# Performance work log

Hardware: AMD Instinct MI355X
Metric: run time of the kernel (lower is better)

The kernel has to match this reference:

```python
import jax, jax.numpy as jnp
import numpy as np

NEG_INF = -1e30
NA_POS = 3  # position of the 'no-answer' token (after [CLS], yes, no)


def mask_pos0(x, mask):
    # keep x where mask==1, set to large negative where mask==0
    return x * mask + (1.0 - mask) * NEG_INF


def make_span_mask(seq_len, max_ans_len):
    m = jnp.tril(jnp.triu(jnp.ones((seq_len, seq_len), jnp.float32), 0), max_ans_len - 1)
    m = m.at[:4, :].set(0.0)
    m = m.at[1, 1].set(1.0)
    m = m.at[2, 2].set(1.0)
    m = m.at[NA_POS, NA_POS].set(1.0)
    return m


def setup_inputs() -> dict:
    key = jax.random.key(0)
    k1, k2, k3 = jax.random.split(key, 3)
    B, S, H = 8, 4096, 1024
    seq_hiddens = jax.random.normal(k1, (B, S, H), jnp.float32)
    ans_mask = jnp.ones((B, S), jnp.float32)
    W_qa = jax.random.normal(k2, (H, 2), jnp.float32) * (1.0 / np.sqrt(H))
    b_qa = jnp.zeros((2,), jnp.float32)
    return {"seq_hiddens": seq_hiddens, "ans_mask": ans_mask, "W_qa": W_qa,
            "b_qa": b_qa, "top_k": 5}


def reference(seq_hiddens, ans_mask, W_qa, b_qa, top_k):
    B, S, H = seq_hiddens.shape
    max_ans_len = 30
    # linear QA head: (B,S,H) @ (H,2) -> (B,S,2)
    span_logits = jnp.einsum('bsh,hc->bsc', seq_hiddens, W_qa) + b_qa
    masked_span_logits = mask_pos0(span_logits, ans_mask[:, :, None])
    start_logits = masked_span_logits[..., 0]  # (B,S)
    end_logits = masked_span_logits[..., 1]    # (B,S)
    # outer-sum span scores: (B,S,S)
    span_scores = start_logits[:, :, None] + end_logits[:, None, :]
    span_mask = make_span_mask(S, max_ans_len)[None]
    masked_span_scores = mask_pos0(span_scores, span_mask)
    flat = masked_span_scores.reshape(B, S * S)
    _, top_span = jax.lax.top_k(flat, top_k)  # (B,k)
    top_start = top_span // S
    top_end = top_span % S
    return start_logits, end_logits, top_start, top_end
```

## Files before the change

kernel.cpp:

```cpp
#include <hip/hip_runtime.h>
#include <cfloat>

#define NEG_INF_F (-1e30f)

__global__ __launch_bounds__(256) void qa_logits_kernel(
    const float* __restrict__ X,
    const float* __restrict__ mask,
    const float* __restrict__ W,
    const float* __restrict__ bqa,
    float* __restrict__ out,
    int total, int H) {
  int wave = (int)((blockIdx.x * (size_t)blockDim.x + threadIdx.x) >> 6);
  int lane = threadIdx.x & 63;
  if (wave >= total) return;
  const float* row = X + (size_t)wave * H;
  float s0 = 0.f, s1 = 0.f;
  int iters = H >> 8;
  for (int k = 0; k < iters; ++k) {
    int h = (k * 64 + lane) * 4;
    const float4 x   = *reinterpret_cast<const float4*>(row + h);
    const float4 w01 = *reinterpret_cast<const float4*>(W + 2 * h);
    const float4 w23 = *reinterpret_cast<const float4*>(W + 2 * h + 4);
    s0 += x.x * w01.x + x.y * w01.z + x.z * w23.x + x.w * w23.z;
    s1 += x.x * w01.y + x.y * w01.w + x.z * w23.y + x.w * w23.w;
  }
#pragma unroll
  for (int off = 32; off > 0; off >>= 1) {
    s0 += __shfl_down(s0, off);
    s1 += __shfl_down(s1, off);
  }
  if (lane == 0) {
    float m = mask[wave];
    float inv = 1.f - m;
    out[wave]         = (s0 + bqa[0]) * m + inv * NEG_INF_F;
    out[total + wave] = (s1 + bqa[1]) * m + inv * NEG_INF_F;
  }
}


__device__ __forceinline__ bool t5_better(float av, int ai, float bv, int bi) {
  return av > bv || (av == bv && ai < bi);
}

__device__ __forceinline__ void t5_insert(float v[5], int id[5], float nv, int ni) {
  if (!t5_better(nv, ni, v[4], id[4])) return;
  v[4] = nv; id[4] = ni;
#pragma unroll
  for (int q = 4; q > 0; --q) {
    if (t5_better(v[q], id[q], v[q - 1], id[q - 1])) {
      float tv = v[q]; v[q] = v[q - 1]; v[q - 1] = tv;
      int ti = id[q]; id[q] = id[q - 1]; id[q - 1] = ti;
    }
  }
}

__device__ __forceinline__ void t5_init(float v[5], int id[5]) {
#pragma unroll
  for (int q = 0; q < 5; ++q) { v[q] = -FLT_MAX; id[q] = 0x7fffffff; }
}

__device__ __forceinline__ void wave_top5(float v[5], int id[5],
                                          float rv[5], int rid[5]) {
#pragma unroll
  for (int r = 0; r < 5; ++r) {
    float bv = v[0]; int bi = id[0];
#pragma unroll
    for (int q = 1; q < 5; ++q)
      if (t5_better(v[q], id[q], bv, bi)) { bv = v[q]; bi = id[q]; }
#pragma unroll
    for (int off = 1; off < 64; off <<= 1) {
      float ov = __shfl_xor(bv, off);
      int oi = __shfl_xor(bi, off);
      if (t5_better(ov, oi, bv, bi)) { bv = ov; bi = oi; }
    }
    rv[r] = bv; rid[r] = bi;
#pragma unroll
    for (int q = 0; q < 5; ++q)
      if (id[q] == bi) v[q] = -FLT_MAX;
  }
}

#define S1_TPB 64

__global__ __launch_bounds__(S1_TPB) void topk_stage1(
    const float* __restrict__ logits,
    float* __restrict__ wv_out,
    int* __restrict__ wi_out,
    int B, int S, int blocks_per_b) {
  int b  = blockIdx.x / blocks_per_b;
  int rb = blockIdx.x % blocks_per_b;
  int lane = (int)threadIdx.x;
  int i = rb * S1_TPB + lane;
  const float* st = logits + (size_t)b * S;
  const float* en = logits + (size_t)(B + b) * S;

  float v[5]; int id[5];
  t5_init(v, id);

  if (i >= 4) {
    float si = st[i];
    float e[30];
#pragma unroll
    for (int c = 0; c < 30; ++c) {
      int j = i + c;
      e[c] = (j < S) ? en[j] : NEG_INF_F;
    }
    int base = i * S + i;
#pragma unroll
    for (int c = 0; c < 30; ++c) t5_insert(v, id, si + e[c], base + c);
  } else if (i >= 1) {
    t5_insert(v, id, st[i] + en[i], i * S + i);
  }

  float rv[5]; int rid[5];
  wave_top5(v, id, rv, rid);

  if (lane == 0) {
    float* ov = wv_out + (size_t)blockIdx.x * 5;
    int*   oi = wi_out + (size_t)blockIdx.x * 5;
#pragma unroll
    for (int q = 0; q < 5; ++q) { ov[q] = rv[q]; oi[q] = rid[q]; }
  }
}

__global__ __launch_bounds__(64) void topk_stage2(
    const float* __restrict__ wv_in, const int* __restrict__ wi_in,
    float* __restrict__ out, int B, int S, int blocks_per_b) {
  int b = blockIdx.x;
  int lane = (int)threadIdx.x;
  int n = blocks_per_b * 5;
  const float* wv = wv_in + (size_t)b * n;
  const int*   wi = wi_in + (size_t)b * n;

  float v[5]; int id[5];
  t5_init(v, id);
#pragma unroll 5
  for (int c = lane; c < n; c += 64)
    t5_insert(v, id, wv[c], wi[c]);

  float rv[5]; int rid[5];
  wave_top5(v, id, rv, rid);

  if (lane == 0) {
    float* ts = out + 2 * (size_t)B * S;
    float* te = ts + (size_t)B * 5;
#pragma unroll
    for (int q = 0; q < 5; ++q) {
      ts[b * 5 + q] = (float)(rid[q] / S);
      te[b * 5 + q] = (float)(rid[q] % S);
    }
  }
}

extern "C" void kernel_launch(void* const* d_in, const int* in_sizes, int n_in,
                              void* d_out, int out_size, void* d_ws, size_t ws_size,
                              hipStream_t stream) {
  const float* X    = (const float*)d_in[0];
  const float* mask = (const float*)d_in[1];
  const float* W    = (const float*)d_in[2];
  const float* bqa  = (const float*)d_in[3];
  const int B = 8, S = 4096, H = 1024;
  const int total = B * S;
  float* out = (float*)d_out;

  int waves_per_block = 256 / 64;
  int blocks = (total + waves_per_block - 1) / waves_per_block;
  qa_logits_kernel<<<blocks, 256, 0, stream>>>(X, mask, W, bqa, out, total, H);

  const int blocks_per_b = S / S1_TPB;
  float* wv_ws = (float*)d_ws;
  int*   wi_ws = (int*)((char*)d_ws + (size_t)B * blocks_per_b * 5 * sizeof(float));
  topk_stage1<<<B * blocks_per_b, S1_TPB, 0, stream>>>(out, wv_ws, wi_ws, B, S, blocks_per_b);
  topk_stage2<<<B, 64, 0, stream>>>(wv_ws, wi_ws, out, B, S, blocks_per_b);
}
```

Measured before the change: 41.77 us.

## Fuse two-stage top-k into one block-per-batch kernel with shared-memory merge

Replaces the two top-k kernels (many small 64-thread blocks writing partials to workspace, then a per-batch merge kernel) with a single kernel of 8 blocks × 1024 threads. Each thread scans four rows, waves reduce, and wave 0 merges the partials through shared memory. The logits kernel is also specialized with compile-time sizes and a fully unrolled inner loop. This saves one launch and the workspace round-trip, but the top-k stage now runs on only 8 workgroups, so it uses far less of the GPU.

```diff
diff --git a/kernel.cpp b/kernel.cpp
--- a/kernel.cpp
+++ b/kernel.cpp
@@ -2,23 +2,26 @@
 #include <cfloat>
 
 #define NEG_INF_F (-1e30f)
+
+constexpr int BB = 8, SS = 4096, HH = 1024;
+constexpr int TOTAL = BB * SS;
+constexpr int MAXLEN = 30;
 
 __global__ __launch_bounds__(256) void qa_logits_kernel(
     const float* __restrict__ X,
     const float* __restrict__ mask,
     const float* __restrict__ W,
     const float* __restrict__ bqa,
-    float* __restrict__ out,
-    int total, int H) {
-  int wave = (int)((blockIdx.x * (size_t)blockDim.x + threadIdx.x) >> 6);
+    float* __restrict__ out) {
+  int row  = (int)((blockIdx.x * (size_t)blockDim.x + threadIdx.x) >> 6);
   int lane = threadIdx.x & 63;
-  if (wave >= total) return;
-  const float* row = X + (size_t)wave * H;
+  if (row >= TOTAL) return;
+  const float* rp = X + (size_t)row * HH;
   float s0 = 0.f, s1 = 0.f;
-  int iters = H >> 8;
-  for (int k = 0; k < iters; ++k) {
+#pragma unroll
+  for (int k = 0; k < HH / 256; ++k) {
     int h = (k * 64 + lane) * 4;
-    const float4 x   = *reinterpret_cast<const float4*>(row + h);
+    const float4 x   = *reinterpret_cast<const float4*>(rp + h);
     const float4 w01 = *reinterpret_cast<const float4*>(W + 2 * h);
     const float4 w23 = *reinterpret_cast<const float4*>(W + 2 * h + 4);
     s0 += x.x * w01.x + x.y * w01.z + x.z * w23.x + x.w * w23.z;
@@ -30,10 +33,10 @@
     s1 += __shfl_down(s1, off);
   }
   if (lane == 0) {
-    float m = mask[wave];
+    float m = mask[row];
     float inv = 1.f - m;
-    out[wave]         = (s0 + bqa[0]) * m + inv * NEG_INF_F;
-    out[total + wave] = (s1 + bqa[1]) * m + inv * NEG_INF_F;
+    out[row]         = (s0 + bqa[0]) * m + inv * NEG_INF_F;
+    out[TOTAL + row] = (s1 + bqa[1]) * m + inv * NEG_INF_F;
   }
 }
 
@@ -80,74 +83,66 @@
   }
 }
 
-#define S1_TPB 64
+#define T2 1024
 
-__global__ __launch_bounds__(S1_TPB) void topk_stage1(
+__global__ __launch_bounds__(T2) void topk_fused(
     const float* __restrict__ logits,
-    float* __restrict__ wv_out,
-    int* __restrict__ wi_out,
-    int B, int S, int blocks_per_b) {
-  int b  = blockIdx.x / blocks_per_b;
-  int rb = blockIdx.x % blocks_per_b;
-  int lane = (int)threadIdx.x;
-  int i = rb * S1_TPB + lane;
-  const float* st = logits + (size_t)b * S;
-  const float* en = logits + (size_t)(B + b) * S;
+    float* __restrict__ out) {
+  const int b = blockIdx.x;
+  const float* st = logits + (size_t)b * SS;
+  const float* en = logits + (size_t)(BB + b) * SS;
+  const int t = (int)threadIdx.x;
+  const int lane = t & 63;
+  const int w = t >> 6;
 
   float v[5]; int id[5];
   t5_init(v, id);
 
-  if (i >= 4) {
-    float si = st[i];
-    float e[30];
 #pragma unroll
-    for (int c = 0; c < 30; ++c) {
-      int j = i + c;
-      e[c] = (j < S) ? en[j] : NEG_INF_F;
+  for (int rr = 0; rr < SS / T2; ++rr) {
+    int i = rr * T2 + t;
+    if (i >= 4) {
+      float si = st[i];
+      float e[MAXLEN];
+#pragma unroll
+      for (int c = 0; c < MAXLEN; ++c) {
+        int j = i + c;
+        e[c] = (j < SS) ? en[j] : NEG_INF_F;
+      }
+      int base = i * SS + i;
+#pragma unroll
+      for (int c = 0; c < MAXLEN; ++c) t5_insert(v, id, si + e[c], base + c);
+    } else if (i >= 1) {
+      t5_insert(v, id, st[i] + en[i], i * SS + i);
     }
-    int base = i * S + i;
-#pragma unroll
-    for (int c = 0; c < 30; ++c) t5_insert(v, id, si + e[c], base + c);
-  } else if (i >= 1) {
-    t5_insert(v, id, st[i] + en[i], i * S + i);
   }
 
   float rv[5]; int rid[5];
   wave_top5(v, id, rv, rid);
 
+  __shared__ float sv[(T2 / 64) * 5];
+  __shared__ int   sid[(T2 / 64) * 5];
   if (lane == 0) {
-    float* ov = wv_out + (size_t)blockIdx.x * 5;
-    int*   oi = wi_out + (size_t)blockIdx.x * 5;
 #pragma unroll
-    for (int q = 0; q < 5; ++q) { ov[q] = rv[q]; oi[q] = rid[q]; }
+    for (int q = 0; q < 5; ++q) { sv[w * 5 + q] = rv[q]; sid[w * 5 + q] = rid[q]; }
   }
-}
+  __syncthreads();
 
-__global__ __launch_bounds__(64) void topk_stage2(
-    const float* __restrict__ wv_in, const int* __restrict__ wi_in,
-    float* __restrict__ out, int B, int S, int blocks_per_b) {
-  int b = blockIdx.x;
-  int lane = (int)threadIdx.x;
-  int n = blocks_per_b * 5;
-  const float* wv = wv_in + (size_t)b * n;
-  const int*   wi = wi_in + (size_t)b * n;
-
-  float v[5]; int id[5];
-  t5_init(v, id);
-#pragma unroll 5
-  for (int c = lane; c < n; c += 64)
-    t5_insert(v, id, wv[c], wi[c]);
-
-  float rv[5]; int rid[5];
-  wave_top5(v, id, rv, rid);
-
-  if (lane == 0) {
-    float* ts = out + 2 * (size_t)B * S;
-    float* te = ts + (size_t)B * 5;
+  if (w == 0) {
+    float fv[5]; int fid[5];
+    t5_init(fv, fid);
+    for (int c = lane; c < (T2 / 64) * 5; c += 64)
+      t5_insert(fv, fid, sv[c], sid[c]);
+    float gv[5]; int gid[5];
+    wave_top5(fv, fid, gv, gid);
+    if (lane == 0) {
+      float* ts = out + 2 * (size_t)TOTAL;
+      float* te = ts + BB * 5;
 #pragma unroll
-    for (int q = 0; q < 5; ++q) {
-      ts[b * 5 + q] = (float)(rid[q] / S);
-      te[b * 5 + q] = (float)(rid[q] % S);
+      for (int q = 0; q < 5; ++q) {
+        ts[b * 5 + q] = (float)(gid[q] >> 12);
+        te[b * 5 + q] = (float)(gid[q] & (SS - 1));
+      }
     }
   }
 }
@@ -159,17 +154,10 @@
   const float* mask = (const float*)d_in[1];
   const float* W    = (const float*)d_in[2];
   const float* bqa  = (const float*)d_in[3];
-  const int B = 8, S = 4096, H = 1024;
-  const int total = B * S;
   float* out = (float*)d_out;
 
-  int waves_per_block = 256 / 64;
-  int blocks = (total + waves_per_block - 1) / waves_per_block;
-  qa_logits_kernel<<<blocks, 256, 0, stream>>>(X, mask, W, bqa, out, total, H);
+  int blocks = TOTAL / 4;
+  qa_logits_kernel<<<blocks, 256, 0, stream>>>(X, mask, W, bqa, out);
 
-  const int blocks_per_b = S / S1_TPB;
-  float* wv_ws = (float*)d_ws;
-  int*   wi_ws = (int*)((char*)d_ws + (size_t)B * blocks_per_b * 5 * sizeof(float));
-  topk_stage1<<<B * blocks_per_b, S1_TPB, 0, stream>>>(out, wv_ws, wi_ws, B, S, blocks_per_b);
-  topk_stage2<<<B, 64, 0, stream>>>(wv_ws, wi_ws, out, B, S, blocks_per_b);
+  topk_fused<<<BB, T2, 0, stream>>>(out, out);
 }
```

Result: slower. 119.7 us (+186.6%).
